# Optimization experiments

Hardware: AMD Instinct MI355X
Metric: run time of the kernel (lower is better)

## Reference

```python
import jax, jax.numpy as jnp
import numpy as np

# Detectron-style RPN GenerateProposals config (cfg[...].RPN_* in the original)
PRE_NMS_TOP_N = 6000
POST_NMS_TOP_N = 1000
NMS_THRESH = 0.7
MIN_SIZE = 16.0
FEAT_STRIDE = 16.0  # 1 / spatial_scale
BBOX_XFORM_CLIP = float(np.log(1000.0 / 16.0))


def _make_anchors():
    # 5 scales x 3 aspect ratios, centered at origin (Detectron-style)
    sizes = [32.0, 64.0, 128.0, 256.0, 512.0]
    ratios = [0.5, 1.0, 2.0]
    out = []
    for s in sizes:
        for r in ratios:
            w = s * np.sqrt(1.0 / r)
            h = s * np.sqrt(r)
            out.append([-(w - 1) / 2.0, -(h - 1) / 2.0, (w - 1) / 2.0, (h - 1) / 2.0])
    return np.asarray(out, dtype=np.float32)  # (15, 4)


def setup_inputs() -> dict:
    key = jax.random.key(0)
    k1, k2 = jax.random.split(key)
    N, A, H, W = 2, 15, 200, 200
    rpn_cls_prob = jax.random.uniform(k1, (N, A, H, W), dtype=jnp.float32)
    rpn_bbox_pred = jax.random.normal(k2, (N, 4 * A, H, W), dtype=jnp.float32) * 0.1
    im_h = H * FEAT_STRIDE
    im_w = W * FEAT_STRIDE
    im_info = jnp.tile(jnp.array([[im_h, im_w, 1.0]], dtype=jnp.float32), (N, 1))
    anchors = jnp.asarray(_make_anchors())
    return {"rpn_cls_prob": rpn_cls_prob, "rpn_bbox_pred": rpn_bbox_pred,
            "im_info": im_info, "anchors": anchors}


def _decode(anchors, deltas):
    # box_utils.bbox_transform with weights (1,1,1,1)
    ws = anchors[:, 2] - anchors[:, 0] + 1.0
    hs = anchors[:, 3] - anchors[:, 1] + 1.0
    cx = anchors[:, 0] + 0.5 * ws
    cy = anchors[:, 1] + 0.5 * hs
    dx, dy = deltas[:, 0], deltas[:, 1]
    dw = jnp.minimum(deltas[:, 2], BBOX_XFORM_CLIP)
    dh = jnp.minimum(deltas[:, 3], BBOX_XFORM_CLIP)
    pcx = dx * ws + cx
    pcy = dy * hs + cy
    pw = jnp.exp(dw) * ws
    ph = jnp.exp(dh) * hs
    return jnp.stack([pcx - 0.5 * pw, pcy - 0.5 * ph,
                      pcx + 0.5 * pw - 1.0, pcy + 0.5 * ph - 1.0], axis=1)


def _iou_matrix(boxes):
    # (P,4) -> (P,P), with +1 convention matching the original numpy code
    x1, y1, x2, y2 = boxes[:, 0], boxes[:, 1], boxes[:, 2], boxes[:, 3]
    areas = (x2 - x1 + 1.0) * (y2 - y1 + 1.0)
    xx1 = jnp.maximum(x1[:, None], x1[None, :])
    yy1 = jnp.maximum(y1[:, None], y1[None, :])
    xx2 = jnp.minimum(x2[:, None], x2[None, :])
    yy2 = jnp.minimum(y2[:, None], y2[None, :])
    iw = jnp.maximum(xx2 - xx1 + 1.0, 0.0)
    ih = jnp.maximum(yy2 - yy1 + 1.0, 0.0)
    inter = iw * ih
    return inter / (areas[:, None] + areas[None, :] - inter)


def _proposals_one_image(scores, deltas, im_info_i, all_anchors):
    # scores: (A,H,W); deltas: (4A,H,W); all_anchors: (K*A,4)
    P = PRE_NMS_TOP_N
    s = scores.transpose(1, 2, 0).reshape(-1)          # (K*A,)
    d = deltas.transpose(1, 2, 0).reshape(-1, 4)       # (K*A,4)
    vals, idx = jax.lax.top_k(s, P)                    # pre-NMS top-k
    props = _decode(all_anchors[idx], d[idx])          # (P,4)
    im_h, im_w, im_scale = im_info_i[0], im_info_i[1], im_info_i[2]
    # clip_tiled_boxes
    x1 = jnp.clip(props[:, 0], 0.0, im_w - 1.0)
    y1 = jnp.clip(props[:, 1], 0.0, im_h - 1.0)
    x2 = jnp.clip(props[:, 2], 0.0, im_w - 1.0)
    y2 = jnp.clip(props[:, 3], 0.0, im_h - 1.0)
    props = jnp.stack([x1, y1, x2, y2], axis=1)
    # _filter_boxes: mask out instead of removing (static shapes)
    min_size = MIN_SIZE * im_scale
    ws = x2 - x1 + 1.0
    hs = y2 - y1 + 1.0
    xc = x1 + ws / 2.0
    yc = y1 + hs / 2.0
    valid = (ws >= min_size) & (hs >= min_size) & (xc < im_w) & (yc < im_h)
    sc = jnp.where(valid, vals, -jnp.inf)
    order = jnp.argsort(-sc)                           # valid boxes first, by score
    props = props[order]
    sc = sc[order]
    valid = valid[order]
    # greedy NMS on score-sorted boxes
    iou = jax.lax.stop_gradient(_iou_matrix(props))    # (P,P)
    pos = jnp.arange(P)

    def step(keep, i):
        sup = (iou[i] > NMS_THRESH) & (pos > i) & keep[i]
        return keep & ~sup, None

    keep, _ = jax.lax.scan(step, valid, jnp.arange(P))
    final_sc = jnp.where(keep, sc, -jnp.inf)
    top_vals, top_idx = jax.lax.top_k(final_sc, POST_NMS_TOP_N)
    ok = jnp.isfinite(top_vals)
    out_props = jnp.where(ok[:, None], props[top_idx], 0.0)
    out_sc = jnp.where(ok, top_vals, 0.0)
    return out_props, out_sc


def reference(rpn_cls_prob, rpn_bbox_pred, im_info, anchors):
    N, A, H, W = rpn_cls_prob.shape
    # anchor shifting: all_anchors (K*A, 4)
    shift_x = jnp.arange(W, dtype=jnp.float32) * FEAT_STRIDE
    shift_y = jnp.arange(H, dtype=jnp.float32) * FEAT_STRIDE
    sx, sy = jnp.meshgrid(shift_x, shift_y)            # 'xy', matches np.meshgrid
    shifts = jnp.stack([sx.ravel(), sy.ravel(), sx.ravel(), sy.ravel()], axis=1)
    all_anchors = (anchors[None, :, :] + shifts[:, None, :]).reshape(-1, 4)
    props, sc = jax.vmap(
        lambda s, d, ii: _proposals_one_image(s, d, ii, all_anchors)
    )(rpn_cls_prob, rpn_bbox_pred, im_info)            # (N,R,4), (N,R)
    R = POST_NMS_TOP_N
    batch_inds = jnp.broadcast_to(
        jnp.arange(N, dtype=jnp.float32)[:, None, None], (N, R, 1))
    rois = jnp.concatenate([batch_inds, props], axis=2).reshape(N * R, 5)
    roi_probs = sc.reshape(N * R, 1)
    # pack [batch_ind, x1, y1, x2, y2, score] into one fixed-shape array
    return jnp.concatenate([rois, roi_probs], axis=1)  # (N*R, 6)
```

## Files before the change

kernel.cpp:

```cpp
#include <hip/hip_runtime.h>
#include <stdint.h>

#define N_IMG 2
#define A_NUM 15
#define HH 200
#define WW 200
#define HW 40000
#define K_TOT 600000
#define K_TOT4 150000
#define P_PRE 6000
#define R_POST 1000
#define NMS_T 0.7f
#define MIN_SZ 16.0f
#define FSTRIDE 16.0f
#define BBOX_CLIP 4.135166556742356f
#define CAND_CAP 8192
#define NWORDS 94
#define BINS 4096
#define MASK_BLOCKS 600
#define ZERO_WORDS (N_IMG * BINS * 2 + N_IMG * 16)
#define MID_T 0.7000000178813934326171875

typedef unsigned long long u64;
typedef uint32_t u32;

__device__ __forceinline__ u32 fkey(float s) {
    return __float_as_uint(s) | 0x80000000u;
}

__device__ __forceinline__ bool iou_gt(float ar, float arj,
                                       const float4& bi, const float4& bj) {
    float xx1 = fmaxf(bi.x, bj.x);
    float yy1 = fmaxf(bi.y, bj.y);
    float xx2 = fminf(bi.z, bj.z);
    float yy2 = fminf(bi.w, bj.w);
    float iw = fmaxf(xx2 - xx1 + 1.0f, 0.0f);
    float ih = fmaxf(yy2 - yy1 + 1.0f, 0.0f);
    float inter = iw * ih;
    float uni = (ar + arj) - inter;
    return (double)inter >= MID_T * (double)uni;
}

__global__ void k_zero(u32* __restrict__ w) {
    int i = blockIdx.x * 1024 + threadIdx.x;
    if (i < ZERO_WORDS) w[i] = 0u;
}

__global__ void k_histA(const float* __restrict__ sc, u32* __restrict__ histA,
                        u32* __restrict__ meta) {
    int n = blockIdx.y;
    __shared__ u32 h[BINS];
    __shared__ u32 part[256];
    __shared__ u32 isLast;
    for (int i = threadIdx.x; i < BINS; i += 256) h[i] = 0;
    __syncthreads();
    const float4* s4 = (const float4*)(sc + (size_t)n * K_TOT);
    for (int i = blockIdx.x * 256 + threadIdx.x; i < K_TOT4; i += 64 * 256) {
        float4 v = s4[i];
        atomicAdd(&h[fkey(v.x) >> 20], 1u);
        atomicAdd(&h[fkey(v.y) >> 20], 1u);
        atomicAdd(&h[fkey(v.z) >> 20], 1u);
        atomicAdd(&h[fkey(v.w) >> 20], 1u);
    }
    __syncthreads();
    for (int i = threadIdx.x; i < BINS; i += 256) {
        u32 v = h[i];
        if (v) atomicAdd(&histA[n * BINS + i], v);
    }
    __threadfence();
    if (threadIdx.x == 0)
        isLast = (atomicAdd(&meta[6], 1u) == (u32)(64 * N_IMG - 1)) ? 1u : 0u;
    __syncthreads();
    if (!isLast) return;
    for (int im = 0; im < N_IMG; ++im) {
        u32* hh = histA + im * BINS;
        u32 s = 0;
        for (int b = threadIdx.x * 16; b < threadIdx.x * 16 + 16; ++b)
            s += atomicAdd(&hh[b], 0u);
        part[threadIdx.x] = s;
        __syncthreads();
        if (threadIdx.x == 0) {
            u32 cum = 0; int seg = 255;
            for (; seg > 0; --seg) {
                if (cum + part[seg] >= P_PRE) break;
                cum += part[seg];
            }
            u32 cgt = cum; int bA = seg * 16; u32 hbA = 0;
            for (int b = seg * 16 + 15; b >= seg * 16; --b) {
                u32 hb = atomicAdd(&hh[b], 0u);
                if (cgt + hb >= P_PRE) { bA = b; hbA = hb; break; }
                cgt += hb;
            }
            meta[im * 16 + 0] = (u32)bA;
            meta[im * 16 + 1] = cgt;
            if (cgt + hbA <= CAND_CAP) {
                meta[im * 16 + 2] = ((u32)bA) << 12;
                meta[im * 16 + 8] = 0u;
            } else {
                meta[im * 16 + 8] = 1u;
            }
        }
        __syncthreads();
    }
}

__global__ void k_histB(const float* __restrict__ sc, u32* __restrict__ histB,
                        u32* __restrict__ meta) {
    int n = blockIdx.y;
    if (meta[n * 16 + 8] == 0u) return;
    __shared__ u32 h[BINS];
    __shared__ u32 part[256];
    __shared__ u32 isLast;
    for (int i = threadIdx.x; i < BINS; i += 256) h[i] = 0;
    __syncthreads();
    u32 bA = meta[n * 16 + 0];
    const float4* s4 = (const float4*)(sc + (size_t)n * K_TOT);
    for (int i = blockIdx.x * 256 + threadIdx.x; i < K_TOT4; i += 64 * 256) {
        float4 v = s4[i];
        u32 k0 = fkey(v.x), k1 = fkey(v.y), k2 = fkey(v.z), k3 = fkey(v.w);
        if ((k0 >> 20) == bA) atomicAdd(&h[(k0 >> 8) & 0xFFFu], 1u);
        if ((k1 >> 20) == bA) atomicAdd(&h[(k1 >> 8) & 0xFFFu], 1u);
        if ((k2 >> 20) == bA) atomicAdd(&h[(k2 >> 8) & 0xFFFu], 1u);
        if ((k3 >> 20) == bA) atomicAdd(&h[(k3 >> 8) & 0xFFFu], 1u);
    }
    __syncthreads();
    for (int i = threadIdx.x; i < BINS; i += 256) {
        u32 v = h[i];
        if (v) atomicAdd(&histB[n * BINS + i], v);
    }
    __threadfence();
    if (threadIdx.x == 0)
        isLast = (atomicAdd(&meta[n * 16 + 7], 1u) == 63u) ? 1u : 0u;
    __syncthreads();
    if (!isLast) return;
    {
        int im = n;
        u32* hh = histB + im * BINS;
        u32 s = 0;
        for (int b = threadIdx.x * 16; b < threadIdx.x * 16 + 16; ++b)
            s += atomicAdd(&hh[b], 0u);
        part[threadIdx.x] = s;
        __syncthreads();
        if (threadIdx.x == 0) {
            u32 cum = meta[im * 16 + 1];
            int seg = 255;
            for (; seg > 0; --seg) {
                if (cum + part[seg] >= P_PRE) break;
                cum += part[seg];
            }
            int bB = seg * 16;
            for (int b = seg * 16 + 15; b >= seg * 16; --b) {
                u32 hb = atomicAdd(&hh[b], 0u);
                if (cum + hb >= P_PRE) { bB = b; break; }
                cum += hb;
            }
            meta[im * 16 + 2] = (meta[im * 16 + 0] << 12) | (u32)bB;
        }
    }
}

__global__ void __launch_bounds__(256) k_compact(const float* __restrict__ sc,
                                                 u32* __restrict__ meta,
                                                 u64* __restrict__ cand) {
    int n = blockIdx.y;
    int tid = threadIdx.x;
    int i4 = blockIdx.x * 256 + tid;
    u32 thr = meta[n * 16 + 2];
    float vv[4] = {0.f, 0.f, 0.f, 0.f};
    u32 flags = 0;
    if (i4 < K_TOT4) {
        const float4* s4 = (const float4*)(sc + (size_t)n * K_TOT);
        float4 v = s4[i4];
        vv[0] = v.x; vv[1] = v.y; vv[2] = v.z; vv[3] = v.w;
        #pragma unroll
        for (int e = 0; e < 4; ++e)
            if ((fkey(vv[e]) >> 8) >= thr) flags |= 1u << e;
    }
    __shared__ u32 scan_[256];
    __shared__ u32 baseS;
    scan_[tid] = __popc(flags);
    __syncthreads();
    for (int off = 1; off < 256; off <<= 1) {
        u32 v = scan_[tid];
        u32 add = (tid >= off) ? scan_[tid - off] : 0u;
        __syncthreads();
        scan_[tid] = v + add;
        __syncthreads();
    }
    if (tid == 255) baseS = atomicAdd(&meta[n * 16 + 3], scan_[255]);
    __syncthreads();
    if (!flags) return;
    u32 pos = baseS + ((tid == 0) ? 0u : scan_[tid - 1]);
    #pragma unroll
    for (int e = 0; e < 4; ++e) {
        if ((flags >> e) & 1u) {
            if (pos < CAND_CAP) {
                int el = i4 * 4 + e;
                int a = el / HW;
                int r = el - a * HW;
                u32 idx = (u32)(r * A_NUM + a);
                cand[n * CAND_CAP + pos] = ((u64)fkey(vv[e]) << 32) | (u32)(~idx);
            }
            pos++;
        }
    }
}

__global__ void __launch_bounds__(256) k_rank(const u64* __restrict__ cand,
                                              const u32* __restrict__ meta,
                                              u32* __restrict__ topk_idx,
                                              float* __restrict__ topk_sc) {
    int n = blockIdx.y;
    u32 cnt = meta[n * 16 + 3];
    if (cnt > CAND_CAP) cnt = CAND_CAP;
    int base = blockIdx.x * 64;
    if (base >= (int)cnt) return;
    __shared__ u64 sk[CAND_CAP];
    __shared__ u32 pr[4][64];
    int tid = threadIdx.x, lane = tid & 63, w = tid >> 6;
    int cntPad = (int)((cnt + 7u) & ~7u);
    const u64* cn = cand + (size_t)n * CAND_CAP;
    for (int i = tid; i < cntPad; i += 256)
        sk[i] = (i < (int)cnt) ? cn[i] : 0ull;
    __syncthreads();
    int myi = base + lane;
    u64 mykey = (myi < (int)cnt) ? sk[myi] : 0ull;
    int stride = ((cntPad >> 2) + 7) & ~7;
    int j0 = w * stride;
    int j1 = min(j0 + stride, cntPad);
    int rank = 0;
    for (int j = j0; j < j1; j += 8) {
        u64 k0 = sk[j + 0], k1 = sk[j + 1], k2 = sk[j + 2], k3 = sk[j + 3];
        u64 k4 = sk[j + 4], k5 = sk[j + 5], k6 = sk[j + 6], k7 = sk[j + 7];
        rank += (int)(k0 > mykey) + (int)(k1 > mykey)
              + (int)(k2 > mykey) + (int)(k3 > mykey)
              + (int)(k4 > mykey) + (int)(k5 > mykey)
              + (int)(k6 > mykey) + (int)(k7 > mykey);
    }
    pr[w][lane] = (u32)rank;
    __syncthreads();
    if (w == 0 && myi < (int)cnt) {
        int r = (int)(pr[0][lane] + pr[1][lane] + pr[2][lane] + pr[3][lane]);
        if (r < P_PRE) {
            topk_idx[n * P_PRE + r] = ~(u32)(mykey & 0xFFFFFFFFull);
            topk_sc[n * P_PRE + r] = __uint_as_float((u32)(mykey >> 32) ^ 0x80000000u);
        }
    }
}

__global__ void k_decode(const u32* __restrict__ topk_idx,
                         const float* __restrict__ bbox, const float* __restrict__ iminfo,
                         const float* __restrict__ anchors,
                         float4* __restrict__ bbox4, u32* __restrict__ bval) {
    int t = blockIdx.x * 256 + threadIdx.x;
    if (t >= N_IMG * P_PRE) return;
    int n = t / P_PRE;
    u32 idx = topk_idx[t];
    int a = (int)(idx % A_NUM);
    int cell = (int)(idx / A_NUM);
    int w = cell % WW, h = cell / WW;
    float ax1 = anchors[a * 4 + 0] + FSTRIDE * (float)w;
    float ay1 = anchors[a * 4 + 1] + FSTRIDE * (float)h;
    float ax2 = anchors[a * 4 + 2] + FSTRIDE * (float)w;
    float ay2 = anchors[a * 4 + 3] + FSTRIDE * (float)h;
    float ws = ax2 - ax1 + 1.0f;
    float hs = ay2 - ay1 + 1.0f;
    float cx = ax1 + 0.5f * ws;
    float cy = ay1 + 0.5f * hs;
    const float* bb = bbox + (size_t)n * 4 * A_NUM * HW + h * WW + w;
    float dx = bb[(4 * a + 0) * HW];
    float dy = bb[(4 * a + 1) * HW];
    float dw = fminf(bb[(4 * a + 2) * HW], BBOX_CLIP);
    float dh = fminf(bb[(4 * a + 3) * HW], BBOX_CLIP);
    float pcx = dx * ws + cx, pcy = dy * hs + cy;
    float pw = expf(dw) * ws, ph = expf(dh) * hs;
    float x1 = pcx - 0.5f * pw;
    float y1 = pcy - 0.5f * ph;
    float x2 = pcx + 0.5f * pw - 1.0f;
    float y2 = pcy + 0.5f * ph - 1.0f;
    float im_h = iminfo[n * 3 + 0], im_w = iminfo[n * 3 + 1], iscale = iminfo[n * 3 + 2];
    x1 = fminf(fmaxf(x1, 0.0f), im_w - 1.0f);
    y1 = fminf(fmaxf(y1, 0.0f), im_h - 1.0f);
    x2 = fminf(fmaxf(x2, 0.0f), im_w - 1.0f);
    y2 = fminf(fmaxf(y2, 0.0f), im_h - 1.0f);
    float wss = x2 - x1 + 1.0f, hss = y2 - y1 + 1.0f;
    float xc = x1 + wss * 0.5f, yc = y1 + hss * 0.5f;
    float ms = MIN_SZ * iscale;
    bool valid = (wss >= ms) && (hss >= ms) && (xc < im_w) && (yc < im_h);
    float4 b; b.x = x1; b.y = y1; b.z = x2; b.w = y2;
    bbox4[t] = b;
    bval[t] = valid ? 1u : 0u;
}

__global__ void __launch_bounds__(1024) k_partition(
        const float4* __restrict__ bbox4,
        const float* __restrict__ bsc, const u32* __restrict__ bval,
        float4* __restrict__ sbox, float* __restrict__ ssc,
        float* __restrict__ sarea, u32* __restrict__ meta) {
    int n = blockIdx.x;
    int t = threadIdx.x;
    __shared__ u32 part[1024];
    int base = t * 6;
    u32 cnt = 0;
    if (base < P_PRE)
        for (int e = 0; e < 6; ++e) cnt += bval[n * P_PRE + base + e];
    part[t] = cnt;
    __syncthreads();
    for (int off = 1; off < 1024; off <<= 1) {
        u32 v = part[t];
        u32 add = (t >= off) ? part[t - off] : 0u;
        __syncthreads();
        part[t] = v + add;
        __syncthreads();
    }
    u32 nv = part[1023];
    u32 excl = (t == 0) ? 0u : part[t - 1];
    if (t == 0) meta[n * 16 + 4] = nv;
    if (base < P_PRE) {
        u32 vseen = excl;
        for (int e = 0; e < 6; ++e) {
            int g = base + e;
            int src = n * P_PRE + g;
            u32 dst;
            if (bval[src]) { dst = vseen; vseen++; }
            else { dst = nv + (u32)g - vseen; }
            int d = n * P_PRE + (int)dst;
            float4 b = bbox4[src];
            sbox[d] = b;
            ssc[d] = bsc[src];
            sarea[d] = (b.z - b.x + 1.0f) * (b.w - b.y + 1.0f);
        }
    }
}

__global__ void __launch_bounds__(256) k_mask(const float4* __restrict__ sbox,
                                              const float* __restrict__ sarea,
                                              u64* __restrict__ mask,
                                              u64* __restrict__ selfmask) {
    int n = blockIdx.y;
    int rem = blockIdx.x;
    int ci = 0;
    while (true) {
        int g = (NWORDS - ci + 7) >> 3;
        if (rem < g) break;
        rem -= g;
        ++ci;
    }
    int cjBase = ci + (rem << 3);
    int lane = threadIdx.x & 63;
    int wv = threadIdx.x >> 6;
    __shared__ float4 sbi[64];
    __shared__ float sar[64];
    const float4* pb = sbox + n * P_PRE;
    const float* pa = sarea + n * P_PRE;
    if (threadIdx.x < 64) {
        int ic = min(ci * 64 + (int)threadIdx.x, P_PRE - 1);
        sbi[threadIdx.x] = pb[ic];
        sar[threadIdx.x] = pa[ic];
    }
    __syncthreads();
    #pragma unroll
    for (int sub = 0; sub < 2; ++sub) {
        int cj = cjBase + wv + sub * 4;
        if (cj >= NWORDS) continue;
        int j = cj * 64 + lane;
        int jc = min(j, P_PRE - 1);
        float4 bj = pb[jc];
        float arj = pa[jc];
        if (cj == ci) {
            u64 sm = 0;
            #pragma unroll 8
            for (int r = 0; r < 64; ++r) {
                bool sup = iou_gt(sar[r], arj, sbi[r], bj) && (r < lane);
                sm |= ((u64)sup) << r;
            }
            if (j < P_PRE) selfmask[(size_t)n * P_PRE + j] = sm;
        } else {
            u64 myword = 0;
            #pragma unroll 8
            for (int r = 0; r < 64; ++r) {
                u64 wrd = __ballot(iou_gt(sar[r], arj, sbi[r], bj));
                if (lane == r) myword = wrd;
            }
            int i = ci * 64 + lane;
            if (i < P_PRE)
                mask[((size_t)n * P_PRE + i) * NWORDS + cj] = myword;
        }
    }
}

__global__ void __launch_bounds__(1024) k_scan(
        const u64* __restrict__ mask, const u64* __restrict__ selfmask,
        const float4* __restrict__ sbox, const float* __restrict__ ssc,
        const u32* __restrict__ meta, float* __restrict__ out) {
    int n = blockIdx.x;
    int tid = threadIdx.x;
    int lane = tid & 63;
    int wv = tid >> 6;
    __shared__ u64 rem[NWORDS];
    __shared__ u64 smb[2][64];
    __shared__ u64 sA;
    __shared__ u32 rowsS[64];
    __shared__ int nkS;
    __shared__ u32 kidx[R_POST];
    __shared__ int keptS;
    u32 nv = meta[n * 16 + 4];
    const u64* mrow = mask + (size_t)n * P_PRE * NWORDS;
    const u64* smk = selfmask + (size_t)n * P_PRE;
    for (int c = tid; c < NWORDS; c += 1024) {
        int b0 = c * 64;
        rem[c] = ((u32)b0 >= nv) ? ~0ull
               : (((u32)(nv - b0) >= 64u) ? 0ull : ((~0ull) << (nv - b0)));
    }
    if (wv == 1) smb[0][lane] = smk[lane];
    if (tid == 0) keptS = 0;
    __syncthreads();
    for (int c = 0; c < NWORDS; ++c) {
        if (wv == 1 && (c + 1) < NWORDS) {
            int j = (c + 1) * 64 + lane;
            smb[(c + 1) & 1][lane] = (j < P_PRE) ? smk[j] : 0ull;
        }
        if (wv == 0) {
            u64 A = ~rem[c];
            if (A) {
                u64 sm = smb[c & 1][lane];
                u64 below = (1ull << lane) - 1ull;
                bool cand = ((A >> lane) & 1ull) != 0ull;
                while (true) {
                    bool sup = (sm & A & below) != 0ull;
                    u64 nA = __ballot(cand && !sup);
                    if (nA == A) break;
                    A = nA;
                }
                int kept = keptS;
                if ((A >> lane) & 1ull) {
                    int rk = (int)__popcll(A & below);
                    int pos = kept + rk;
                    if (pos < R_POST) kidx[pos] = (u32)(c * 64 + lane);
                    rowsS[rk] = (u32)lane;
                }
                if (lane == 0) {
                    keptS = kept + (int)__popcll(A);
                    nkS = (int)__popcll(A);
                    sA = A;
                }
            } else if (lane == 0) { sA = 0; nkS = 0; }
        }
        __syncthreads();
        if (keptS >= R_POST) break;
        if (sA) {
            int colSlot = tid & 127;
            int rg = tid >> 7;
            int col = c + 1 + colSlot;
            int nk = nkS;
            if (col < NWORDS && rg < nk) {
                int jbase = c * 64;
                u64 acc = 0;
                for (int r = rg; r < nk; r += 32) {
                    int r1 = r + 8, r2 = r + 16, r3 = r + 24;
                    u64 v0 = mrow[(size_t)(jbase + (int)rowsS[r]) * NWORDS + col];
                    u64 v1 = (r1 < nk) ? mrow[(size_t)(jbase + (int)rowsS[r1]) * NWORDS + col] : 0ull;
                    u64 v2 = (r2 < nk) ? mrow[(size_t)(jbase + (int)rowsS[r2]) * NWORDS + col] : 0ull;
                    u64 v3 = (r3 < nk) ? mrow[(size_t)(jbase + (int)rowsS[r3]) * NWORDS + col] : 0ull;
                    acc |= v0 | v1 | v2 | v3;
                }
                if (acc) atomicOr(&rem[col], acc);
            }
        }
        __syncthreads();
    }
    __syncthreads();
    int kept = keptS;
    for (int r = tid; r < R_POST; r += 1024) {
        float4 b = make_float4(0.f, 0.f, 0.f, 0.f);
        float s = 0.f;
        if (r < kept) {
            u32 i = kidx[r];
            b = sbox[n * P_PRE + (int)i];
            s = ssc[n * P_PRE + (int)i];
        }
        float* o = out + (size_t)(n * R_POST + r) * 6;
        o[0] = (float)n;
        o[1] = b.x; o[2] = b.y; o[3] = b.z; o[4] = b.w; o[5] = s;
    }
}

extern "C" void kernel_launch(void* const* d_in, const int* in_sizes, int n_in,
                              void* d_out, int out_size, void* d_ws, size_t ws_size,
                              hipStream_t stream) {
    const float* scores  = (const float*)d_in[0];
    const float* bbox    = (const float*)d_in[1];
    const float* iminfo  = (const float*)d_in[2];
    const float* anchors = (const float*)d_in[3];
    float* out = (float*)d_out;

    char* ws = (char*)d_ws;
    size_t off = 0;
    u32* histA = (u32*)(ws + off); off += (size_t)N_IMG * BINS * 4;
    u32* histB = (u32*)(ws + off); off += (size_t)N_IMG * BINS * 4;
    u32* meta  = (u32*)(ws + off); off += (size_t)N_IMG * 16 * 4;
    u64* cand      = (u64*)(ws + off);   off += (size_t)N_IMG * CAND_CAP * 8;
    u32* topk_idx  = (u32*)(ws + off);   off += (size_t)N_IMG * P_PRE * 4;
    float* topk_sc = (float*)(ws + off); off += (size_t)N_IMG * P_PRE * 4;
    float4* bbox4 = (float4*)(ws + off); off += (size_t)N_IMG * P_PRE * 16;
    u32* bval  = (u32*)(ws + off);       off += (size_t)N_IMG * P_PRE * 4;
    float4* sbox = (float4*)(ws + off);  off += (size_t)N_IMG * P_PRE * 16;
    float* ssc = (float*)(ws + off);     off += (size_t)N_IMG * P_PRE * 4;
    float* sarea = (float*)(ws + off);   off += (size_t)N_IMG * P_PRE * 4;
    u64* selfmask = (u64*)(ws + off);    off += (size_t)N_IMG * P_PRE * 8;
    u64* mask = (u64*)(ws + off);        off += (size_t)N_IMG * P_PRE * NWORDS * 8;
    (void)ws_size; (void)in_sizes; (void)n_in; (void)out_size;

    k_zero<<<(ZERO_WORDS + 1023) / 1024, 1024, 0, stream>>>((u32*)d_ws);

    dim3 gHist(64, N_IMG);
    k_histA<<<gHist, 256, 0, stream>>>(scores, histA, meta);
    k_histB<<<gHist, 256, 0, stream>>>(scores, histB, meta);
    dim3 gComp((K_TOT4 + 255) / 256, N_IMG);
    k_compact<<<gComp, 256, 0, stream>>>(scores, meta, cand);
    dim3 gRank(CAND_CAP / 64, N_IMG);
    k_rank<<<gRank, 256, 0, stream>>>(cand, meta, topk_idx, topk_sc);
    k_decode<<<(N_IMG * P_PRE + 255) / 256, 256, 0, stream>>>(topk_idx, bbox, iminfo,
                                                              anchors, bbox4, bval);
    k_partition<<<N_IMG, 1024, 0, stream>>>(bbox4, topk_sc, bval, sbox, ssc, sarea, meta);
    dim3 gMask(MASK_BLOCKS, N_IMG);
    k_mask<<<gMask, 256, 0, stream>>>(sbox, sarea, mask, selfmask);
    k_scan<<<N_IMG, 1024, 0, stream>>>(mask, selfmask, sbox, ssc, meta, out);
}
```

Before: 167.9 us.

## Fuse rank and decode kernels; use wavefront shuffle scans in compact/partition

After: 164.4 us. -2.1%, faster.

```diff
diff --git a/kernel.cpp b/kernel.cpp
--- a/kernel.cpp
+++ b/kernel.cpp
@@ -164,6 +164,7 @@
                                                  u64* __restrict__ cand) {
     int n = blockIdx.y;
     int tid = threadIdx.x;
+    int lane = tid & 63, w = tid >> 6;
     int i4 = blockIdx.x * 256 + tid;
     u32 thr = meta[n * 16 + 2];
     float vv[4] = {0.f, 0.f, 0.f, 0.f};
@@ -176,21 +177,26 @@
         for (int e = 0; e < 4; ++e)
             if ((fkey(vv[e]) >> 8) >= thr) flags |= 1u << e;
     }
-    __shared__ u32 scan_[256];
+    u32 cnt = (u32)__popc(flags);
+    u32 incl = cnt;
+    #pragma unroll
+    for (int off = 1; off < 64; off <<= 1) {
+        u32 v = __shfl_up(incl, (unsigned)off);
+        if (lane >= off) incl += v;
+    }
+    __shared__ u32 wtot[4];
     __shared__ u32 baseS;
-    scan_[tid] = __popc(flags);
-    __syncthreads();
-    for (int off = 1; off < 256; off <<= 1) {
-        u32 v = scan_[tid];
-        u32 add = (tid >= off) ? scan_[tid - off] : 0u;
-        __syncthreads();
-        scan_[tid] = v + add;
-        __syncthreads();
-    }
-    if (tid == 255) baseS = atomicAdd(&meta[n * 16 + 3], scan_[255]);
+    if (lane == 63) wtot[w] = incl;
+    __syncthreads();
+    if (tid == 0) {
+        u32 tot = wtot[0] + wtot[1] + wtot[2] + wtot[3];
+        baseS = atomicAdd(&meta[n * 16 + 3], tot);
+    }
     __syncthreads();
     if (!flags) return;
-    u32 pos = baseS + ((tid == 0) ? 0u : scan_[tid - 1]);
+    u32 wbase = 0;
+    for (int i = 0; i < w; ++i) wbase += wtot[i];
+    u32 pos = baseS + wbase + (incl - cnt);
     #pragma unroll
     for (int e = 0; e < 4; ++e) {
         if ((flags >> e) & 1u) {
@@ -206,10 +212,12 @@
     }
 }
 
-__global__ void __launch_bounds__(256) k_rank(const u64* __restrict__ cand,
-                                              const u32* __restrict__ meta,
-                                              u32* __restrict__ topk_idx,
-                                              float* __restrict__ topk_sc) {
+__global__ void __launch_bounds__(256) k_rankdec(
+        const u64* __restrict__ cand, const u32* __restrict__ meta,
+        const float* __restrict__ bbox, const float* __restrict__ iminfo,
+        const float* __restrict__ anchors,
+        float* __restrict__ topk_sc, float4* __restrict__ bbox4,
+        u32* __restrict__ bval) {
     int n = blockIdx.y;
     u32 cnt = meta[n * 16 + 3];
     if (cnt > CAND_CAP) cnt = CAND_CAP;
@@ -239,35 +247,24 @@
     }
     pr[w][lane] = (u32)rank;
     __syncthreads();
-    if (w == 0 && myi < (int)cnt) {
-        int r = (int)(pr[0][lane] + pr[1][lane] + pr[2][lane] + pr[3][lane]);
-        if (r < P_PRE) {
-            topk_idx[n * P_PRE + r] = ~(u32)(mykey & 0xFFFFFFFFull);
-            topk_sc[n * P_PRE + r] = __uint_as_float((u32)(mykey >> 32) ^ 0x80000000u);
-        }
-    }
-}
-
-__global__ void k_decode(const u32* __restrict__ topk_idx,
-                         const float* __restrict__ bbox, const float* __restrict__ iminfo,
-                         const float* __restrict__ anchors,
-                         float4* __restrict__ bbox4, u32* __restrict__ bval) {
-    int t = blockIdx.x * 256 + threadIdx.x;
-    if (t >= N_IMG * P_PRE) return;
-    int n = t / P_PRE;
-    u32 idx = topk_idx[t];
+    if (w != 0 || myi >= (int)cnt) return;
+    int r = (int)(pr[0][lane] + pr[1][lane] + pr[2][lane] + pr[3][lane]);
+    if (r >= P_PRE) return;
+    u32 idx = ~(u32)(mykey & 0xFFFFFFFFull);
+    float score = __uint_as_float((u32)(mykey >> 32) ^ 0x80000000u);
+    topk_sc[n * P_PRE + r] = score;
     int a = (int)(idx % A_NUM);
     int cell = (int)(idx / A_NUM);
-    int w = cell % WW, h = cell / WW;
-    float ax1 = anchors[a * 4 + 0] + FSTRIDE * (float)w;
-    float ay1 = anchors[a * 4 + 1] + FSTRIDE * (float)h;
-    float ax2 = anchors[a * 4 + 2] + FSTRIDE * (float)w;
-    float ay2 = anchors[a * 4 + 3] + FSTRIDE * (float)h;
+    int ww = cell % WW, hh = cell / WW;
+    float ax1 = anchors[a * 4 + 0] + FSTRIDE * (float)ww;
+    float ay1 = anchors[a * 4 + 1] + FSTRIDE * (float)hh;
+    float ax2 = anchors[a * 4 + 2] + FSTRIDE * (float)ww;
+    float ay2 = anchors[a * 4 + 3] + FSTRIDE * (float)hh;
     float ws = ax2 - ax1 + 1.0f;
     float hs = ay2 - ay1 + 1.0f;
     float cx = ax1 + 0.5f * ws;
     float cy = ay1 + 0.5f * hs;
-    const float* bb = bbox + (size_t)n * 4 * A_NUM * HW + h * WW + w;
+    const float* bb = bbox + (size_t)n * 4 * A_NUM * HW + hh * WW + ww;
     float dx = bb[(4 * a + 0) * HW];
     float dy = bb[(4 * a + 1) * HW];
     float dw = fminf(bb[(4 * a + 2) * HW], BBOX_CLIP);
@@ -288,8 +285,8 @@
     float ms = MIN_SZ * iscale;
     bool valid = (wss >= ms) && (hss >= ms) && (xc < im_w) && (yc < im_h);
     float4 b; b.x = x1; b.y = y1; b.z = x2; b.w = y2;
-    bbox4[t] = b;
-    bval[t] = valid ? 1u : 0u;
+    bbox4[n * P_PRE + r] = b;
+    bval[n * P_PRE + r] = valid ? 1u : 0u;
 }
 
 __global__ void __launch_bounds__(1024) k_partition(
@@ -299,22 +296,28 @@
         float* __restrict__ sarea, u32* __restrict__ meta) {
     int n = blockIdx.x;
     int t = threadIdx.x;
-    __shared__ u32 part[1024];
+    int lane = t & 63, w = t >> 6;
     int base = t * 6;
     u32 cnt = 0;
     if (base < P_PRE)
         for (int e = 0; e < 6; ++e) cnt += bval[n * P_PRE + base + e];
-    part[t] = cnt;
-    __syncthreads();
-    for (int off = 1; off < 1024; off <<= 1) {
-        u32 v = part[t];
-        u32 add = (t >= off) ? part[t - off] : 0u;
-        __syncthreads();
-        part[t] = v + add;
-        __syncthreads();
-    }
-    u32 nv = part[1023];
-    u32 excl = (t == 0) ? 0u : part[t - 1];
+    u32 incl = cnt;
+    #pragma unroll
+    for (int off = 1; off < 64; off <<= 1) {
+        u32 v = __shfl_up(incl, (unsigned)off);
+        if (lane >= off) incl += v;
+    }
+    __shared__ u32 wtot[16];
+    if (lane == 63) wtot[w] = incl;
+    __syncthreads();
+    u32 nv = 0, wbase = 0;
+    #pragma unroll
+    for (int i = 0; i < 16; ++i) {
+        u32 x = wtot[i];
+        if (i < w) wbase += x;
+        nv += x;
+    }
+    u32 excl = wbase + (incl - cnt);
     if (t == 0) meta[n * 16 + 4] = nv;
     if (base < P_PRE) {
         u32 vseen = excl;
@@ -500,7 +503,6 @@
     u32* histB = (u32*)(ws + off); off += (size_t)N_IMG * BINS * 4;
     u32* meta  = (u32*)(ws + off); off += (size_t)N_IMG * 16 * 4;
     u64* cand      = (u64*)(ws + off);   off += (size_t)N_IMG * CAND_CAP * 8;
-    u32* topk_idx  = (u32*)(ws + off);   off += (size_t)N_IMG * P_PRE * 4;
     float* topk_sc = (float*)(ws + off); off += (size_t)N_IMG * P_PRE * 4;
     float4* bbox4 = (float4*)(ws + off); off += (size_t)N_IMG * P_PRE * 16;
     u32* bval  = (u32*)(ws + off);       off += (size_t)N_IMG * P_PRE * 4;
@@ -519,9 +521,8 @@
     dim3 gComp((K_TOT4 + 255) / 256, N_IMG);
     k_compact<<<gComp, 256, 0, stream>>>(scores, meta, cand);
     dim3 gRank(CAND_CAP / 64, N_IMG);
-    k_rank<<<gRank, 256, 0, stream>>>(cand, meta, topk_idx, topk_sc);
-    k_decode<<<(N_IMG * P_PRE + 255) / 256, 256, 0, stream>>>(topk_idx, bbox, iminfo,
-                                                              anchors, bbox4, bval);
+    k_rankdec<<<gRank, 256, 0, stream>>>(cand, meta, bbox, iminfo, anchors,
+                                         topk_sc, bbox4, bval);
     k_partition<<<N_IMG, 1024, 0, stream>>>(bbox4, topk_sc, bval, sbox, ssc, sarea, meta);
     dim3 gMask(MASK_BLOCKS, N_IMG);
     k_mask<<<gMask, 256, 0, stream>>>(sbox, sarea, mask, selfmask);
```
